# Kernel optimization log

Measured on AMD Instinct MI355X. Metric: run time of the kernel, lower is better.

## Reference

```python
import jax, jax.numpy as jnp
import numpy as np

NUM_NODES = 2048
NUM_REL = 8
HIDDEN = 256


def setup_inputs() -> dict:
    key = jax.random.key(0)
    k1, k2, k3 = jax.random.split(key, 3)
    X = jax.random.normal(k1, (NUM_NODES, HIDDEN, NUM_REL), dtype=jnp.float32)
    A = jax.random.uniform(k2, (NUM_NODES, NUM_NODES, NUM_REL), dtype=jnp.float32)
    # nn.init.normal_(std=0.01)
    weight = 0.01 * jax.random.normal(k3, (HIDDEN, HIDDEN, NUM_REL), dtype=jnp.float32)
    return {"X": X, "A": A, "weight": weight}


def _tensor_product(A, B):
    # Faithful to the original: FFT along last (relation) dim, take REAL part of
    # both transformed operands, per-slice matmul, then real part of ifft.
    Af = jnp.real(jnp.fft.fft(A, axis=-1))  # (n1, n2, k)
    Bf = jnp.real(jnp.fft.fft(B, axis=-1))  # (n2, n4, k)
    C = jnp.einsum('nmk,mhk->nhk', Af, Bf)  # batched real matmul over slices k
    return jnp.real(jnp.fft.ifft(C, axis=-1)).astype(A.dtype)


def reference(X, A, weight):
    res = _tensor_product(A, X)          # (num_nodes, hidden, num_rel)
    res = _tensor_product(res, weight)   # (num_nodes, hidden, num_rel)
    return res
```

## Files before the change

### kernel.cpp

```cpp
#include <hip/hip_runtime.h>


typedef __bf16 bf16_t;
typedef __bf16 bf16x2 __attribute__((ext_vector_type(2)));
typedef __bf16 bf16x8 __attribute__((ext_vector_type(8)));
typedef float f32x4 __attribute__((ext_vector_type(4)));

#define R2C 0.70710678118654752f

__device__ __forceinline__ size_t swz(int r, int c, int K) {
  return (size_t)r * K + (c & ~63) + ((((c >> 3) & 7) ^ (r & 7)) << 3) + (c & 7);
}

__device__ __forceinline__ void async_cp16(const void* g, void* l) {
  __builtin_amdgcn_global_load_lds((const __attribute__((address_space(1))) char*)g,
                                   (__attribute__((address_space(3))) char*)l,
                                   16, 0, 0);
}

__device__ __forceinline__ void fwd5(const float x[8], float F[5]) {
  float s04 = x[0] + x[4], d04 = x[0] - x[4];
  float s26 = x[2] + x[6];
  float s15 = x[1] + x[5], s37 = x[3] + x[7];
  float t = (x[1] + x[7]) - (x[3] + x[5]);
  float e = s04 + s26, o = s15 + s37;
  F[0] = e + o;
  F[1] = d04 + R2C * t;
  F[2] = s04 - s26;
  F[3] = d04 - R2C * t;
  F[4] = e - o;
}

__global__ __launch_bounds__(256) void k_pre(const float* __restrict__ X,
                                             const float* __restrict__ A,
                                             const float* __restrict__ W,
                                             bf16_t* __restrict__ Xft,
                                             bf16_t* __restrict__ Af,
                                             bf16_t* __restrict__ Wft) {
  __shared__ bf16_t tx[40][256];
  int b = blockIdx.x;
  if (b < 8192) {
    size_t t = (size_t)b * 256 + threadIdx.x;
    size_t idx = t * 2;
    int n = (int)(idx >> 11), m = (int)(idx & 2047);
    const float4* p = (const float4*)(A + idx * 8);
    float4 q0 = p[0], q1 = p[1], q2 = p[2], q3 = p[3];
    float x0[8] = {q0.x, q0.y, q0.z, q0.w, q1.x, q1.y, q1.z, q1.w};
    float x1[8] = {q2.x, q2.y, q2.z, q2.w, q3.x, q3.y, q3.z, q3.w};
    float F0[5], F1[5];
    fwd5(x0, F0);
    fwd5(x1, F1);
    size_t pos = swz(n, m, 2048);
#pragma unroll
    for (int j = 0; j < 5; j++) {
      bf16x2 v = {(bf16_t)F0[j], (bf16_t)F1[j]};
      *(bf16x2*)(Af + (size_t)j * 4194304 + pos) = v;
    }
  } else if (b < 8448) {
    int bx = b - 8192;
    int m0 = (bx & 7) * 256, h0 = (bx >> 3) * 8;
    int t = threadIdx.x;
    const float4* p = (const float4*)(X + (((size_t)(m0 + t) * 256) + h0) * 8);
#pragma unroll
    for (int h = 0; h < 8; h++) {
      float4 a = p[2 * h], bb = p[2 * h + 1];
      float x[8] = {a.x, a.y, a.z, a.w, bb.x, bb.y, bb.z, bb.w};
      float F[5];
      fwd5(x, F);
#pragma unroll
      for (int j = 0; j < 5; j++) tx[j * 8 + h][t] = (bf16_t)F[j];
    }
    __syncthreads();
#pragma unroll
    for (int it = 0; it < 5; it++) {
      int slot = it * 256 + t;
      int row = slot >> 5, ch = slot & 31;
      int j = row >> 3, hl = row & 7;
      int h = h0 + hl;
      size_t gpos = (size_t)j * 524288 + (size_t)h * 2048 + m0 +
                    ((ch & ~7) << 3) + (((ch & 7) ^ (h & 7)) << 3);
      *(uint4*)(Xft + gpos) = *(const uint4*)(&tx[row][ch * 8]);
    }
  } else {
    int h = b - 8448;
    int hp = threadIdx.x;
    const float4* p = (const float4*)(W + ((size_t)hp * 256 + h) * 8);
    float4 a = p[0], bb = p[1];
    float x[8] = {a.x, a.y, a.z, a.w, bb.x, bb.y, bb.z, bb.w};
    float F[5];
    fwd5(x, F);
    const float sc[5] = {0.125f, 0.25f, 0.25f, 0.25f, 0.125f};
    size_t pos = swz(h, hp, 256);
#pragma unroll
    for (int j = 0; j < 5; j++)
      Wft[(size_t)j * 65536 + pos] = (bf16_t)(F[j] * sc[j]);
  }
}

template <typename OutT, bool SWZ_OUT>
__global__ __launch_bounds__(256) void gemm_lds(const bf16_t* __restrict__ A,
                                                const bf16_t* __restrict__ B,
                                                OutT* __restrict__ C, int K,
                                                size_t ap, size_t bp, size_t cp) {
  __shared__ bf16_t sm[4 * 8192];
  const int j = blockIdx.z;
  const bf16_t* Aj = A + (size_t)j * ap;
  const bf16_t* Bj = B + (size_t)j * bp;
  OutT* Cj = C + (size_t)j * cp;
  const int n0 = blockIdx.x * 128, h0 = blockIdx.y * 128;
  const int tid = threadIdx.x;
  const int wv = tid >> 6, ln = tid & 63;
  const int quad = ln >> 4, l16 = ln & 15;
  const int wn = (wv & 1) * 64, wh = (wv >> 1) * 64;

  const bf16_t* ga[4];
  const bf16_t* gb[4];
  int lo[4];
#pragma unroll
  for (int s = 0; s < 4; s++) {
    int slot = s * 256 + tid;
    int row = slot >> 3, c16 = slot & 7;
    ga[s] = Aj + (size_t)(n0 + row) * K + c16 * 8;
    gb[s] = Bj + (size_t)(h0 + row) * K + c16 * 8;
    lo[s] = (s * 256 + wv * 64) * 8;
  }

#pragma unroll
  for (int s = 0; s < 4; s++) {
    async_cp16(ga[s], sm + lo[s]);
    async_cp16(gb[s], sm + 16384 + lo[s]);
  }

  f32x4 acc[4][4] = {};
  for (int kk = 0; kk < K; kk += 64) {
    int p = (kk >> 6) & 1;
    if (kk + 64 < K) {
#pragma unroll
      for (int s = 0; s < 4; s++) {
        async_cp16(ga[s] + kk + 64, sm + (p ^ 1) * 8192 + lo[s]);
        async_cp16(gb[s] + kk + 64, sm + 16384 + (p ^ 1) * 8192 + lo[s]);
      }
      __builtin_amdgcn_s_waitcnt(0xF78);
    } else {
      __builtin_amdgcn_s_waitcnt(0xF70);
    }
    __builtin_amdgcn_s_barrier();
    const bf16_t* Asp = sm + p * 8192;
    const bf16_t* Bsp = sm + 16384 + p * 8192;
#pragma unroll
    for (int kh = 0; kh < 2; kh++) {
      bf16x8 af[4], bfr[4];
      int c16 = kh * 4 + quad;
#pragma unroll
      for (int i = 0; i < 4; i++) {
        int ra = wn + i * 16 + l16;
        int rb = wh + i * 16 + l16;
        af[i] = *(const bf16x8*)(Asp + ra * 64 + ((c16 ^ (ra & 7)) << 3));
        bfr[i] = *(const bf16x8*)(Bsp + rb * 64 + ((c16 ^ (rb & 7)) << 3));
      }
#pragma unroll
      for (int i = 0; i < 4; i++)
#pragma unroll
        for (int t = 0; t < 4; t++)
          acc[i][t] = __builtin_amdgcn_mfma_f32_16x16x32_bf16(af[i], bfr[t],
                                                              acc[i][t], 0, 0, 0);
    }
    __builtin_amdgcn_s_barrier();
  }
#pragma unroll
  for (int i = 0; i < 4; i++) {
#pragma unroll
    for (int t = 0; t < 4; t++) {
      int hc = h0 + wh + t * 16 + l16;
#pragma unroll
      for (int rg = 0; rg < 4; rg++) {
        int nr = n0 + wn + i * 16 + quad * 4 + rg;
        size_t off = SWZ_OUT ? swz(nr, hc, 256) : (size_t)nr * 256 + hc;
        Cj[off] = (OutT)acc[i][t][rg];
      }
    }
  }
}

__global__ __launch_bounds__(256) void k_combine(const float* __restrict__ C2,
                                                 float* __restrict__ out) {
  size_t idx = (size_t)blockIdx.x * 256 + threadIdx.x;
  float c0 = C2[idx];
  float c1 = C2[524288 + idx];
  float c2 = C2[2 * 524288 + idx];
  float c3 = C2[3 * 524288 + idx];
  float c4 = C2[4 * 524288 + idx];
  float o0 = c0 + c1 + c2 + c3 + c4;
  float o4 = c0 - c1 + c2 - c3 + c4;
  float o2 = c0 - c2 + c4;
  float rt = R2C * (c1 - c3);
  float o1 = c0 + rt - c4;
  float o3 = c0 - rt - c4;
  float4* op = (float4*)(out + idx * 8);
  op[0] = make_float4(o0, o1, o2, o3);
  op[1] = make_float4(o4, o3, o2, o1);
}

extern "C" void kernel_launch(void* const* d_in, const int* in_sizes, int n_in,
                              void* d_out, int out_size, void* d_ws, size_t ws_size,
                              hipStream_t stream) {
  const float* X = (const float*)d_in[0];
  const float* A = (const float*)d_in[1];
  const float* W = (const float*)d_in[2];
  float* out = (float*)d_out;
  char* ws = (char*)d_ws;

  bf16_t* Af  = (bf16_t*)(ws);
  bf16_t* Xft = (bf16_t*)(ws + 41943040);
  bf16_t* Wft = (bf16_t*)(ws + 47185920);
  bf16_t* C1  = (bf16_t*)(ws + 47841280);
  float*  C2  = (float*) (ws + 53084160);

  k_pre<<<dim3(8704), 256, 0, stream>>>(X, A, W, Xft, Af, Wft);
  gemm_lds<bf16_t, true><<<dim3(16, 2, 5), 256, 0, stream>>>(
      Af, Xft, C1, 2048, (size_t)4194304, (size_t)524288, (size_t)524288);
  gemm_lds<float, false><<<dim3(16, 2, 5), 256, 0, stream>>>(
      C1, Wft, C2, 256, (size_t)524288, (size_t)65536, (size_t)524288);
  k_combine<<<dim3(2048), 256, 0, stream>>>(C2, out);
}
```

Measured before the change: 256.1 us.

## Widen A-FFT prepass to 8 elements per thread and halve GEMM1 tile height

The A forward-FFT prepass now has each thread handle 8 consecutive (n,m) entries. It reads them with nontemporal vector loads and writes one 16-byte bf16x8 store per frequency slice instead of 4-byte stores, which cuts store transactions and the block count. The first GEMM is templated on the B-tile height and launched with 64-wide H tiles. That doubles its grid from 160 to 320 blocks to fill more of the GPU's compute units, at the cost of more A-tile reloads. Each thread in the prepass now keeps more live registers.

```diff
diff --git a/kernel.cpp b/kernel.cpp
--- a/kernel.cpp
+++ b/kernel.cpp
@@ -39,25 +39,29 @@
                                              bf16_t* __restrict__ Wft) {
   __shared__ bf16_t tx[40][256];
   int b = blockIdx.x;
-  if (b < 8192) {
+  if (b < 2048) {
     size_t t = (size_t)b * 256 + threadIdx.x;
-    size_t idx = t * 2;
-    int n = (int)(idx >> 11), m = (int)(idx & 2047);
-    const float4* p = (const float4*)(A + idx * 8);
-    float4 q0 = p[0], q1 = p[1], q2 = p[2], q3 = p[3];
-    float x0[8] = {q0.x, q0.y, q0.z, q0.w, q1.x, q1.y, q1.z, q1.w};
-    float x1[8] = {q2.x, q2.y, q2.z, q2.w, q3.x, q3.y, q3.z, q3.w};
-    float F0[5], F1[5];
-    fwd5(x0, F0);
-    fwd5(x1, F1);
-    size_t pos = swz(n, m, 2048);
+    size_t idx = t * 8;
+    int n = (int)(idx >> 11), m8 = (int)(idx & 2047);
+    const f32x4* p = (const f32x4*)(A + idx * 8);
+    float F[8][5];
+#pragma unroll
+    for (int u = 0; u < 8; u++) {
+      f32x4 a = __builtin_nontemporal_load(p + 2 * u);
+      f32x4 bb = __builtin_nontemporal_load(p + 2 * u + 1);
+      float x[8] = {a.x, a.y, a.z, a.w, bb.x, bb.y, bb.z, bb.w};
+      fwd5(x, F[u]);
+    }
+    size_t pos = (size_t)n * 2048 + (m8 & ~63) + ((((m8 >> 3) & 7) ^ (n & 7)) << 3);
 #pragma unroll
     for (int j = 0; j < 5; j++) {
-      bf16x2 v = {(bf16_t)F0[j], (bf16_t)F1[j]};
-      *(bf16x2*)(Af + (size_t)j * 4194304 + pos) = v;
-    }
-  } else if (b < 8448) {
-    int bx = b - 8192;
+      bf16x8 v = {(bf16_t)F[0][j], (bf16_t)F[1][j], (bf16_t)F[2][j],
+                  (bf16_t)F[3][j], (bf16_t)F[4][j], (bf16_t)F[5][j],
+                  (bf16_t)F[6][j], (bf16_t)F[7][j]};
+      *(bf16x8*)(Af + (size_t)j * 4194304 + pos) = v;
+    }
+  } else if (b < 2304) {
+    int bx = b - 2048;
     int m0 = (bx & 7) * 256, h0 = (bx >> 3) * 8;
     int t = threadIdx.x;
     const float4* p = (const float4*)(X + (((size_t)(m0 + t) * 256) + h0) * 8);
@@ -82,7 +86,7 @@
       *(uint4*)(Xft + gpos) = *(const uint4*)(&tx[row][ch * 8]);
     }
   } else {
-    int h = b - 8448;
+    int h = b - 2304;
     int hp = threadIdx.x;
     const float4* p = (const float4*)(W + ((size_t)hp * 256 + h) * 8);
     float4 a = p[0], bb = p[1];
@@ -97,71 +101,86 @@
   }
 }
 
-template <typename OutT, bool SWZ_OUT>
+template <typename OutT, bool SWZ_OUT, int BH>
 __global__ __launch_bounds__(256) void gemm_lds(const bf16_t* __restrict__ A,
                                                 const bf16_t* __restrict__ B,
                                                 OutT* __restrict__ C, int K,
                                                 size_t ap, size_t bp, size_t cp) {
-  __shared__ bf16_t sm[4 * 8192];
+  constexpr int WH = BH / 2;
+  constexpr int NT = WH / 16;
+  constexpr int BR = BH / 32;
+  constexpr int ABUF = 128 * 64;
+  constexpr int BBUF = BH * 64;
+  __shared__ bf16_t sm[2 * ABUF + 2 * BBUF];
   const int j = blockIdx.z;
   const bf16_t* Aj = A + (size_t)j * ap;
   const bf16_t* Bj = B + (size_t)j * bp;
   OutT* Cj = C + (size_t)j * cp;
-  const int n0 = blockIdx.x * 128, h0 = blockIdx.y * 128;
+  const int n0 = blockIdx.x * 128, h0 = blockIdx.y * BH;
   const int tid = threadIdx.x;
   const int wv = tid >> 6, ln = tid & 63;
   const int quad = ln >> 4, l16 = ln & 15;
-  const int wn = (wv & 1) * 64, wh = (wv >> 1) * 64;
+  const int wn = (wv & 1) * 64, wh = (wv >> 1) * WH;
 
   const bf16_t* ga[4];
-  const bf16_t* gb[4];
-  int lo[4];
+  int loA[4];
 #pragma unroll
   for (int s = 0; s < 4; s++) {
     int slot = s * 256 + tid;
     int row = slot >> 3, c16 = slot & 7;
     ga[s] = Aj + (size_t)(n0 + row) * K + c16 * 8;
+    loA[s] = (s * 256 + wv * 64) * 8;
+  }
+  const bf16_t* gb[BR];
+  int loB[BR];
+#pragma unroll
+  for (int s = 0; s < BR; s++) {
+    int slot = s * 256 + tid;
+    int row = slot >> 3, c16 = slot & 7;
     gb[s] = Bj + (size_t)(h0 + row) * K + c16 * 8;
-    lo[s] = (s * 256 + wv * 64) * 8;
-  }
-
-#pragma unroll
-  for (int s = 0; s < 4; s++) {
-    async_cp16(ga[s], sm + lo[s]);
-    async_cp16(gb[s], sm + 16384 + lo[s]);
-  }
-
-  f32x4 acc[4][4] = {};
+    loB[s] = (s * 256 + wv * 64) * 8;
+  }
+
+#pragma unroll
+  for (int s = 0; s < 4; s++) async_cp16(ga[s], sm + loA[s]);
+#pragma unroll
+  for (int s = 0; s < BR; s++) async_cp16(gb[s], sm + 2 * ABUF + loB[s]);
+
+  f32x4 acc[4][NT] = {};
   for (int kk = 0; kk < K; kk += 64) {
     int p = (kk >> 6) & 1;
     if (kk + 64 < K) {
 #pragma unroll
-      for (int s = 0; s < 4; s++) {
-        async_cp16(ga[s] + kk + 64, sm + (p ^ 1) * 8192 + lo[s]);
-        async_cp16(gb[s] + kk + 64, sm + 16384 + (p ^ 1) * 8192 + lo[s]);
-      }
-      __builtin_amdgcn_s_waitcnt(0xF78);
+      for (int s = 0; s < 4; s++)
+        async_cp16(ga[s] + kk + 64, sm + (p ^ 1) * ABUF + loA[s]);
+#pragma unroll
+      for (int s = 0; s < BR; s++)
+        async_cp16(gb[s] + kk + 64, sm + 2 * ABUF + (p ^ 1) * BBUF + loB[s]);
+      __builtin_amdgcn_s_waitcnt(0xF70 | (4 + BR));
     } else {
       __builtin_amdgcn_s_waitcnt(0xF70);
     }
     __builtin_amdgcn_s_barrier();
-    const bf16_t* Asp = sm + p * 8192;
-    const bf16_t* Bsp = sm + 16384 + p * 8192;
+    const bf16_t* Asp = sm + p * ABUF;
+    const bf16_t* Bsp = sm + 2 * ABUF + p * BBUF;
 #pragma unroll
     for (int kh = 0; kh < 2; kh++) {
-      bf16x8 af[4], bfr[4];
+      bf16x8 af[4], bfr[NT];
       int c16 = kh * 4 + quad;
 #pragma unroll
       for (int i = 0; i < 4; i++) {
         int ra = wn + i * 16 + l16;
-        int rb = wh + i * 16 + l16;
         af[i] = *(const bf16x8*)(Asp + ra * 64 + ((c16 ^ (ra & 7)) << 3));
-        bfr[i] = *(const bf16x8*)(Bsp + rb * 64 + ((c16 ^ (rb & 7)) << 3));
       }
 #pragma unroll
+      for (int t = 0; t < NT; t++) {
+        int rb = wh + t * 16 + l16;
+        bfr[t] = *(const bf16x8*)(Bsp + rb * 64 + ((c16 ^ (rb & 7)) << 3));
+      }
+#pragma unroll
       for (int i = 0; i < 4; i++)
 #pragma unroll
-        for (int t = 0; t < 4; t++)
+        for (int t = 0; t < NT; t++)
           acc[i][t] = __builtin_amdgcn_mfma_f32_16x16x32_bf16(af[i], bfr[t],
                                                               acc[i][t], 0, 0, 0);
     }
@@ -170,7 +189,7 @@
 #pragma unroll
   for (int i = 0; i < 4; i++) {
 #pragma unroll
-    for (int t = 0; t < 4; t++) {
+    for (int t = 0; t < NT; t++) {
       int hc = h0 + wh + t * 16 + l16;
 #pragma unroll
       for (int rg = 0; rg < 4; rg++) {
@@ -216,10 +235,10 @@
   bf16_t* C1  = (bf16_t*)(ws + 47841280);
   float*  C2  = (float*) (ws + 53084160);
 
-  k_pre<<<dim3(8704), 256, 0, stream>>>(X, A, W, Xft, Af, Wft);
-  gemm_lds<bf16_t, true><<<dim3(16, 2, 5), 256, 0, stream>>>(
+  k_pre<<<dim3(2560), 256, 0, stream>>>(X, A, W, Xft, Af, Wft);
+  gemm_lds<bf16_t, true, 64><<<dim3(16, 4, 5), 256, 0, stream>>>(
       Af, Xft, C1, 2048, (size_t)4194304, (size_t)524288, (size_t)524288);
-  gemm_lds<float, false><<<dim3(16, 2, 5), 256, 0, stream>>>(
+  gemm_lds<float, false, 128><<<dim3(16, 2, 5), 256, 0, stream>>>(
       C1, Wft, C2, 256, (size_t)524288, (size_t)65536, (size_t)524288);
   k_combine<<<dim3(2048), 256, 0, stream>>>(C2, out);
 }
```

After: 277.6 us. 8.4% more time.
